# Kernel tuning notes

Hardware: AMD Instinct MI355X
Metric: run time of the kernel (lower is better)

Reference implementation:

```python
import jax, jax.numpy as jnp
import numpy as np

HID = 128


def setup_inputs() -> dict:
    key = jax.random.key(0)
    ks = jax.random.split(key, 7)
    B = 131072
    X = jax.random.normal(ks[0], (B, 4), dtype=jnp.float32)
    # Linear params stored as (in, out); scaled ~ 1/sqrt(fan_in) like torch default
    W1 = jax.random.normal(ks[1], (4, HID), dtype=jnp.float32) * 0.5
    b1 = jnp.zeros((HID,), jnp.float32)
    W2 = jax.random.normal(ks[2], (HID, HID), dtype=jnp.float32) * (1.0 / np.sqrt(HID))
    b2 = jnp.zeros((HID,), jnp.float32)
    W3 = jax.random.normal(ks[3], (HID, 1), dtype=jnp.float32) * (1.0 / np.sqrt(HID))
    b3 = jnp.zeros((1,), jnp.float32)
    return {"X": X, "W1": W1, "b1": b1, "W2": W2, "b2": b2, "W3": W3, "b3": b3}


def reference(X, W1, b1, W2, b2, W3, b3):
    def V_fn(feat):  # feat: [4] -> scalar potential
        h = jnp.tanh(feat @ W1 + b1)
        h = jnp.tanh(h @ W2 + b2)
        return (h @ W3 + b3)[0]

    def L_single(q, qd):  # q:[2], qd:[2] -> scalar Lagrangian
        t1, t2 = q[0], q[1]
        w1, w2 = qd[0], qd[1]
        T = w1 ** 2 + 0.5 * w2 ** 2 + w1 * w2 * jnp.cos(t1 - t2)
        feat = jnp.stack([jnp.sin(t1), jnp.cos(t1), jnp.sin(t2), jnp.cos(t2)])
        return T - V_fn(feat)

    q = X[:, :2]
    qd = X[:, 2:]
    dL_dq = jax.vmap(jax.grad(L_single, argnums=0))(q, qd)          # [B,2]
    # mass matrix M[i,j] = d^2 L / (d qd_i d qd_j)
    M = jax.vmap(jax.jacfwd(jax.grad(L_single, argnums=1), argnums=1))(q, qd)  # [B,2,2]
    # cross Hessian H[i,j] = d^2 L / (d qd_i d q_j); Coriolis C_i = H[i,:] @ qd
    H = jax.vmap(jax.jacfwd(jax.grad(L_single, argnums=1), argnums=0))(q, qd)  # [B,2,2]
    C = jnp.einsum('bij,bj->bi', H, qd)                              # [B,2]
    qdd = jnp.linalg.solve(M, (dL_dq - C)[..., None])[..., 0]        # [B,2]
    return jnp.concatenate([qd, qdd], axis=1)                        # [B,4]
```

## Files before the change

kernel.cpp:

```cpp
#include <hip/hip_runtime.h>
#include <math.h>

#define HID 128
#define SPB 64
#define TPB 512
#define GRIDB 512

typedef __bf16 bf16;
typedef bf16 bf16x8 __attribute__((ext_vector_type(8)));
typedef bf16 bf16x4 __attribute__((ext_vector_type(4)));
typedef float floatx4 __attribute__((ext_vector_type(4)));

__device__ __forceinline__ float fast_tanh(float x) {
    float e = __builtin_amdgcn_exp2f(x * 2.885390081777927f);
    return 1.0f - 2.0f * __builtin_amdgcn_rcpf(e + 1.0f);
}


__global__ __launch_bounds__(TPB, 4)
void lnn_kernel(const float* __restrict__ X,
                const float* __restrict__ W1,
                const float* __restrict__ b1,
                const float* __restrict__ b2,
                const float* __restrict__ W3,
                const float* __restrict__ W2,
                float* __restrict__ out,
                int B, int nchunk)
{
    __shared__ __align__(16) bf16 sW2A[16384];
    __shared__ __align__(16) bf16 sH1 [8192];
    __shared__ __align__(16) bf16 sG2 [8192];
    __shared__ __align__(16) float4 sW1c[HID];
    __shared__ float sB1[HID], sB2[HID], sW3[HID];
    __shared__ __align__(16) float sFeat[2][SPB][4];
    __shared__ float sQd[2][SPB][2];
    __shared__ __align__(16) float sDV[4][SPB][4];

    const int tid  = threadIdx.x;
    const int w    = tid >> 6;
    const int lane = tid & 63;
    const int lrow = lane & 15;
    const int lq   = lane >> 4;
    const int wlo  = w & 3;
    const int whi  = w >> 2;

    if (tid < HID) {
        sW1c[tid] = make_float4(W1[tid], W1[HID + tid], W1[2*HID + tid], W1[3*HID + tid]);
        sB1[tid]  = b1[tid];
    } else if (tid < 2 * HID) {
        sB2[tid - HID] = b2[tid - HID];
        sW3[tid - HID] = W3[tid - HID];
    }
    #pragma unroll
    for (int tt = 0; tt < 4; ++tt) {
        int e = tid + tt * TPB;
        int t = e >> 6, l = e & 63;
        int jt = t >> 2, kt = t & 3;
        int lr = l & 15, q = l >> 4;
        bf16x8 f;
        #pragma unroll
        for (int idx = 0; idx < 8; ++idx)
            f[idx] = (bf16)W2[(32*kt + 8*q + idx) * HID + 16*jt + lr];
        *reinterpret_cast<bf16x8*>(&sW2A[e * 8]) = f;
    }
    bf16x8 bW1 = {};
    if (lrow < 4) {
        const float4* wp = reinterpret_cast<const float4*>(&W1[lrow*HID + 32*wlo + 8*lq]);
        float4 a = wp[0], b = wp[1];
        bW1[0]=(bf16)a.x; bW1[1]=(bf16)a.y; bW1[2]=(bf16)a.z; bW1[3]=(bf16)a.w;
        bW1[4]=(bf16)b.x; bW1[5]=(bf16)b.y; bW1[6]=(bf16)b.z; bW1[7]=(bf16)b.w;
    }
    bf16x8 aW2[2][4];
    #pragma unroll
    for (int u = 0; u < 2; ++u) {
        const float* rbase = &W2[(16*(2*wlo + u) + lrow) * HID + 8*lq];
        #pragma unroll
        for (int jt2 = 0; jt2 < 4; ++jt2) {
            const float4* rp = reinterpret_cast<const float4*>(rbase + 32*jt2);
            float4 r0 = rp[0], r1 = rp[1];
            bf16x8 g;
            g[0]=(bf16)r0.x; g[1]=(bf16)r0.y; g[2]=(bf16)r0.z; g[3]=(bf16)r0.w;
            g[4]=(bf16)r1.x; g[5]=(bf16)r1.y; g[6]=(bf16)r1.z; g[7]=(bf16)r1.w;
            aW2[u][jt2] = g;
        }
    }
    if (tid >= TPB - SPB) {
        int s  = tid - (TPB - SPB);
        int g  = (int)blockIdx.x * SPB + s;
        int gc = g < B ? g : (B - 1);
        float4 x = reinterpret_cast<const float4*>(X)[gc];
        float s1, c1, s2, c2;
        __sincosf(x.x, &s1, &c1);
        __sincosf(x.y, &s2, &c2);
        sFeat[0][s][0]=s1; sFeat[0][s][1]=c1; sFeat[0][s][2]=s2; sFeat[0][s][3]=c2;
        sQd[0][s][0]=x.z;  sQd[0][s][1]=x.w;
    }
    __syncthreads();

    #pragma unroll 1
    for (int c = 0; c < nchunk; ++c) {
        const int par = c & 1;
        const int s0  = (c * GRIDB + (int)blockIdx.x) * SPB;

        {
            int s = 16 * wlo + lrow;
            float f0 = sFeat[par][s][0], f1 = sFeat[par][s][1];
            float f2 = sFeat[par][s][2], f3 = sFeat[par][s][3];
            #pragma unroll
            for (int h = 0; h < 2; ++h) {
                int kt = 2 * whi + h;
                int jb = 32 * kt + 8 * lq;
                float4 t0 = *reinterpret_cast<const float4*>(&sB1[jb]);
                float4 t1 = *reinterpret_cast<const float4*>(&sB1[jb + 4]);
                float bias[8] = {t0.x,t0.y,t0.z,t0.w,t1.x,t1.y,t1.z,t1.w};
                bf16x8 hf;
                #pragma unroll
                for (int idx = 0; idx < 8; ++idx) {
                    float4 wc = sW1c[jb + idx];
                    float z = bias[idx] + f0*wc.x + f1*wc.y + f2*wc.z + f3*wc.w;
                    hf[idx] = (bf16)fast_tanh(z);
                }
                *reinterpret_cast<bf16x8*>(&sH1[((wlo*4 + kt)*64 + lane)*8]) = hf;
            }
        }
        __syncthreads();

        floatx4 acc[2][2];
        #pragma unroll
        for (int t = 0; t < 2; ++t)
            #pragma unroll
            for (int s = 0; s < 2; ++s) acc[t][s] = floatx4{0.f,0.f,0.f,0.f};
        #pragma unroll
        for (int kt = 0; kt < 4; ++kt) {
            bf16x8 a0 = *reinterpret_cast<const bf16x8*>(&sW2A[(((2*wlo  )*4 + kt)*64 + lane)*8]);
            bf16x8 a1 = *reinterpret_cast<const bf16x8*>(&sW2A[(((2*wlo+1)*4 + kt)*64 + lane)*8]);
            bf16x8 b0 = *reinterpret_cast<const bf16x8*>(&sH1 [(((2*whi  )*4 + kt)*64 + lane)*8]);
            bf16x8 b1 = *reinterpret_cast<const bf16x8*>(&sH1 [(((2*whi+1)*4 + kt)*64 + lane)*8]);
            acc[0][0] = __builtin_amdgcn_mfma_f32_16x16x32_bf16(a0, b0, acc[0][0], 0,0,0);
            acc[0][1] = __builtin_amdgcn_mfma_f32_16x16x32_bf16(a0, b1, acc[0][1], 0,0,0);
            acc[1][0] = __builtin_amdgcn_mfma_f32_16x16x32_bf16(a1, b0, acc[1][0], 0,0,0);
            acc[1][1] = __builtin_amdgcn_mfma_f32_16x16x32_bf16(a1, b1, acc[1][1], 0,0,0);
        }

        #pragma unroll
        for (int t = 0; t < 2; ++t) {
            int jb = 16*(2*wlo + t) + 4*lq;
            float4 b2v = *reinterpret_cast<const float4*>(&sB2[jb]);
            float4 w3v = *reinterpret_cast<const float4*>(&sW3[jb]);
            float bbv[4] = {b2v.x, b2v.y, b2v.z, b2v.w};
            float w3a[4] = {w3v.x, w3v.y, w3v.z, w3v.w};
            int q2  = 2*t + (lq >> 1);
            int sub = 4 * (lq & 1);
            #pragma unroll
            for (int s = 0; s < 2; ++s) {
                int st = 2*whi + s;
                bf16x4 g;
                #pragma unroll
                for (int r = 0; r < 4; ++r) {
                    float h = fast_tanh(acc[t][s][r] + bbv[r]);
                    g[r] = (bf16)((1.0f - h*h) * w3a[r]);
                }
                *reinterpret_cast<bf16x4*>(&sG2[((st*4 + wlo)*64 + (q2*16 + lrow))*8 + sub]) = g;
            }
        }
        __syncthreads();

        #pragma unroll
        for (int t = 0; t < 2; ++t)
            #pragma unroll
            for (int s = 0; s < 2; ++s) acc[t][s] = floatx4{0.f,0.f,0.f,0.f};
        #pragma unroll
        for (int jt2 = 0; jt2 < 4; ++jt2) {
            bf16x8 g0 = *reinterpret_cast<const bf16x8*>(&sG2[(((2*whi  )*4 + jt2)*64 + lane)*8]);
            bf16x8 g1 = *reinterpret_cast<const bf16x8*>(&sG2[(((2*whi+1)*4 + jt2)*64 + lane)*8]);
            acc[0][0] = __builtin_amdgcn_mfma_f32_16x16x32_bf16(aW2[0][jt2], g0, acc[0][0], 0,0,0);
            acc[0][1] = __builtin_amdgcn_mfma_f32_16x16x32_bf16(aW2[0][jt2], g1, acc[0][1], 0,0,0);
            acc[1][0] = __builtin_amdgcn_mfma_f32_16x16x32_bf16(aW2[1][jt2], g0, acc[1][0], 0,0,0);
            acc[1][1] = __builtin_amdgcn_mfma_f32_16x16x32_bf16(aW2[1][jt2], g1, acc[1][1], 0,0,0);
        }

        #pragma unroll
        for (int u = 0; u < 2; ++u) {
            int q2  = 2*u + (lq >> 1);
            int sub = 4 * (lq & 1);
            #pragma unroll
            for (int s = 0; s < 2; ++s) {
                int st  = 2*whi + s;
                int off = ((st*4 + wlo)*64 + (q2*16 + lrow))*8 + sub;
                bf16x4 h4 = *reinterpret_cast<const bf16x4*>(&sH1[off]);
                bf16x4 g;
                #pragma unroll
                for (int r = 0; r < 4; ++r) {
                    float h1 = (float)h4[r];
                    g[r] = (bf16)((1.0f - h1*h1) * acc[u][s][r]);
                }
                *reinterpret_cast<bf16x4*>(&sH1[off]) = g;
            }
        }

        if (tid >= TPB - SPB && c + 1 < nchunk) {
            int s  = tid - (TPB - SPB);
            int g  = ((c + 1) * GRIDB + (int)blockIdx.x) * SPB + s;
            int gc = g < B ? g : (B - 1);
            float4 x = reinterpret_cast<const float4*>(X)[gc];
            float s1, c1, s2, c2;
            __sincosf(x.x, &s1, &c1);
            __sincosf(x.y, &s2, &c2);
            int np = par ^ 1;
            sFeat[np][s][0]=s1; sFeat[np][s][1]=c1; sFeat[np][s][2]=s2; sFeat[np][s][3]=c2;
            sQd[np][s][0]=x.z;  sQd[np][s][1]=x.w;
        }

        {
            bf16x8 g0 = *reinterpret_cast<const bf16x8*>(&sH1[(((2*whi  )*4 + wlo)*64 + lane)*8]);
            bf16x8 g1 = *reinterpret_cast<const bf16x8*>(&sH1[(((2*whi+1)*4 + wlo)*64 + lane)*8]);
            floatx4 d0 = __builtin_amdgcn_mfma_f32_16x16x32_bf16(bW1, g0, floatx4{0.f,0.f,0.f,0.f}, 0,0,0);
            floatx4 d1 = __builtin_amdgcn_mfma_f32_16x16x32_bf16(bW1, g1, floatx4{0.f,0.f,0.f,0.f}, 0,0,0);
            if (lane < 16) {
                *reinterpret_cast<float4*>(&sDV[wlo][16*(2*whi  ) + lane][0]) =
                    make_float4(d0[0], d0[1], d0[2], d0[3]);
                *reinterpret_cast<float4*>(&sDV[wlo][16*(2*whi+1) + lane][0]) =
                    make_float4(d1[0], d1[1], d1[2], d1[3]);
            }
        }
        __syncthreads();

        if (tid < SPB) {
            int g = s0 + tid;
            if (g < B) {
                float4 d0 = *reinterpret_cast<const float4*>(&sDV[0][tid][0]);
                float4 d1 = *reinterpret_cast<const float4*>(&sDV[1][tid][0]);
                float4 d2 = *reinterpret_cast<const float4*>(&sDV[2][tid][0]);
                float4 d3 = *reinterpret_cast<const float4*>(&sDV[3][tid][0]);
                float dV0 = d0.x + d1.x + d2.x + d3.x;
                float dV1 = d0.y + d1.y + d2.y + d3.y;
                float dV2 = d0.z + d1.z + d2.z + d3.z;
                float dV3 = d0.w + d1.w + d2.w + d3.w;
                float s1 = sFeat[par][tid][0], c1 = sFeat[par][tid][1];
                float s2 = sFeat[par][tid][2], c2 = sFeat[par][tid][3];
                float w1 = sQd[par][tid][0],  w2 = sQd[par][tid][1];
                float cosD = c1 * c2 + s1 * s2;
                float sinD = s1 * c2 - c1 * s2;
                float dVt1 = dV0 * c1 - dV1 * s1;
                float dVt2 = dV2 * c2 - dV3 * s2;
                float sT = w1 * w2 * sinD;
                float cw = sinD * (w2 - w1);
                float rhs1 = (-sT - dVt1) - w2 * cw;
                float rhs2 = ( sT - dVt2) - w1 * cw;
                float det = 2.0f - cosD * cosD;
                float inv = __builtin_amdgcn_rcpf(det);
                float qdd1 = (rhs1 - cosD * rhs2) * inv;
                float qdd2 = (2.0f * rhs2 - cosD * rhs1) * inv;
                *reinterpret_cast<float4*>(&out[4 * g]) = make_float4(w1, w2, qdd1, qdd2);
            }
        }
    }
}

extern "C" void kernel_launch(void* const* d_in, const int* in_sizes, int n_in,
                              void* d_out, int out_size, void* d_ws, size_t ws_size,
                              hipStream_t stream) {
    const float* X  = (const float*)d_in[0];
    const float* W1 = (const float*)d_in[1];
    const float* b1 = (const float*)d_in[2];
    const float* W2 = (const float*)d_in[3];
    const float* b2 = (const float*)d_in[4];
    const float* W3 = (const float*)d_in[5];
    float* out = (float*)d_out;
    int B = in_sizes[0] / 4;
    int nchunk = (B + GRIDB * SPB - 1) / (GRIDB * SPB);
    lnn_kernel<<<GRIDB, TPB, 0, stream>>>(X, W1, b1, b2, W3, W2, out, B, nchunk);
}
```

Baseline: 91.62 us.

## Hold W2 forward tiles in registers, alias LDS buffers, raise grid and occupancy

The transposed W2 A-fragments are loaded from LDS into registers once before the chunk loop, and the staging region is then reused for the H1 and G2 buffers, roughly halving shared-memory use. That makes room for a larger grid (768 blocks) and a launch_bounds minimum of 6 blocks per CU, which should improve latency hiding. W1 is stored row-major so the layer-1 and tanh work can be expressed as float4 vector operations. The risk is register pressure: 16 bf16x8 weight fragments held per thread under a tighter register cap could cause spills.

```diff
diff --git a/kernel.cpp b/kernel.cpp
--- a/kernel.cpp
+++ b/kernel.cpp
@@ -4,20 +4,25 @@
 #define HID 128
 #define SPB 64
 #define TPB 512
-#define GRIDB 512
+#define GRIDB 768
 
 typedef __bf16 bf16;
 typedef bf16 bf16x8 __attribute__((ext_vector_type(8)));
 typedef bf16 bf16x4 __attribute__((ext_vector_type(4)));
 typedef float floatx4 __attribute__((ext_vector_type(4)));
 
-__device__ __forceinline__ float fast_tanh(float x) {
-    float e = __builtin_amdgcn_exp2f(x * 2.885390081777927f);
-    return 1.0f - 2.0f * __builtin_amdgcn_rcpf(e + 1.0f);
+__device__ __forceinline__ floatx4 tanh4(floatx4 z) {
+    floatx4 t = z * 2.885390081777927f;
+    floatx4 e = { __builtin_amdgcn_exp2f(t[0]), __builtin_amdgcn_exp2f(t[1]),
+                  __builtin_amdgcn_exp2f(t[2]), __builtin_amdgcn_exp2f(t[3]) };
+    e = e + 1.0f;
+    floatx4 r = { __builtin_amdgcn_rcpf(e[0]), __builtin_amdgcn_rcpf(e[1]),
+                  __builtin_amdgcn_rcpf(e[2]), __builtin_amdgcn_rcpf(e[3]) };
+    return 1.0f - 2.0f * r;
 }
 
 
-__global__ __launch_bounds__(TPB, 4)
+__global__ __launch_bounds__(TPB, 6)
 void lnn_kernel(const float* __restrict__ X,
                 const float* __restrict__ W1,
                 const float* __restrict__ b1,
@@ -27,14 +32,15 @@
                 float* __restrict__ out,
                 int B, int nchunk)
 {
-    __shared__ __align__(16) bf16 sW2A[16384];
-    __shared__ __align__(16) bf16 sH1 [8192];
-    __shared__ __align__(16) bf16 sG2 [8192];
-    __shared__ __align__(16) float4 sW1c[HID];
-    __shared__ float sB1[HID], sB2[HID], sW3[HID];
+    __shared__ __align__(16) bf16 sBuf[16384];
+    __shared__ __align__(16) float sW1r[4][HID];
+    __shared__ __align__(16) float sB1[HID], sB2[HID], sW3[HID];
     __shared__ __align__(16) float sFeat[2][SPB][4];
     __shared__ float sQd[2][SPB][2];
     __shared__ __align__(16) float sDV[4][SPB][4];
+
+    bf16* const sH1 = sBuf;
+    bf16* const sG2 = sBuf + 8192;
 
     const int tid  = threadIdx.x;
     const int w    = tid >> 6;
@@ -44,13 +50,14 @@
     const int wlo  = w & 3;
     const int whi  = w >> 2;
 
-    if (tid < HID) {
-        sW1c[tid] = make_float4(W1[tid], W1[HID + tid], W1[2*HID + tid], W1[3*HID + tid]);
-        sB1[tid]  = b1[tid];
-    } else if (tid < 2 * HID) {
-        sB2[tid - HID] = b2[tid - HID];
-        sW3[tid - HID] = W3[tid - HID];
-    }
+    {
+        int r = tid >> 7, j = tid & (HID - 1);
+        sW1r[r][j] = W1[r * HID + j];
+    }
+    if (tid < HID) sB1[tid] = b1[tid];
+    else if (tid < 2 * HID) sB2[tid - HID] = b2[tid - HID];
+    else if (tid < 3 * HID) sW3[tid - 2 * HID] = W3[tid - 2 * HID];
+
     #pragma unroll
     for (int tt = 0; tt < 4; ++tt) {
         int e = tid + tt * TPB;
@@ -61,7 +68,7 @@
         #pragma unroll
         for (int idx = 0; idx < 8; ++idx)
             f[idx] = (bf16)W2[(32*kt + 8*q + idx) * HID + 16*jt + lr];
-        *reinterpret_cast<bf16x8*>(&sW2A[e * 8]) = f;
+        *reinterpret_cast<bf16x8*>(&sBuf[e * 8]) = f;
     }
     bf16x8 bW1 = {};
     if (lrow < 4) {
@@ -97,6 +104,14 @@
     }
     __syncthreads();
 
+    bf16x8 aW2T[2][4];
+    #pragma unroll
+    for (int u = 0; u < 2; ++u)
+        #pragma unroll
+        for (int kt = 0; kt < 4; ++kt)
+            aW2T[u][kt] = *reinterpret_cast<const bf16x8*>(&sBuf[(((2*wlo+u)*4 + kt)*64 + lane)*8]);
+    __syncthreads();
+
     #pragma unroll 1
     for (int c = 0; c < nchunk; ++c) {
         const int par = c & 1;
@@ -110,16 +125,23 @@
             for (int h = 0; h < 2; ++h) {
                 int kt = 2 * whi + h;
                 int jb = 32 * kt + 8 * lq;
-                float4 t0 = *reinterpret_cast<const float4*>(&sB1[jb]);
-                float4 t1 = *reinterpret_cast<const float4*>(&sB1[jb + 4]);
-                float bias[8] = {t0.x,t0.y,t0.z,t0.w,t1.x,t1.y,t1.z,t1.w};
+                floatx4 w0a = *reinterpret_cast<const floatx4*>(&sW1r[0][jb]);
+                floatx4 w0b = *reinterpret_cast<const floatx4*>(&sW1r[0][jb+4]);
+                floatx4 w1a = *reinterpret_cast<const floatx4*>(&sW1r[1][jb]);
+                floatx4 w1b = *reinterpret_cast<const floatx4*>(&sW1r[1][jb+4]);
+                floatx4 w2a = *reinterpret_cast<const floatx4*>(&sW1r[2][jb]);
+                floatx4 w2b = *reinterpret_cast<const floatx4*>(&sW1r[2][jb+4]);
+                floatx4 w3a = *reinterpret_cast<const floatx4*>(&sW1r[3][jb]);
+                floatx4 w3b = *reinterpret_cast<const floatx4*>(&sW1r[3][jb+4]);
+                floatx4 bba = *reinterpret_cast<const floatx4*>(&sB1[jb]);
+                floatx4 bbb = *reinterpret_cast<const floatx4*>(&sB1[jb+4]);
+                floatx4 za = bba + f0*w0a + f1*w1a + f2*w2a + f3*w3a;
+                floatx4 zb = bbb + f0*w0b + f1*w1b + f2*w2b + f3*w3b;
+                floatx4 ha = tanh4(za);
+                floatx4 hb = tanh4(zb);
                 bf16x8 hf;
-                #pragma unroll
-                for (int idx = 0; idx < 8; ++idx) {
-                    float4 wc = sW1c[jb + idx];
-                    float z = bias[idx] + f0*wc.x + f1*wc.y + f2*wc.z + f3*wc.w;
-                    hf[idx] = (bf16)fast_tanh(z);
-                }
+                hf[0]=(bf16)ha[0]; hf[1]=(bf16)ha[1]; hf[2]=(bf16)ha[2]; hf[3]=(bf16)ha[3];
+                hf[4]=(bf16)hb[0]; hf[5]=(bf16)hb[1]; hf[6]=(bf16)hb[2]; hf[7]=(bf16)hb[3];
                 *reinterpret_cast<bf16x8*>(&sH1[((wlo*4 + kt)*64 + lane)*8]) = hf;
             }
         }
@@ -132,34 +154,28 @@
             for (int s = 0; s < 2; ++s) acc[t][s] = floatx4{0.f,0.f,0.f,0.f};
         #pragma unroll
         for (int kt = 0; kt < 4; ++kt) {
-            bf16x8 a0 = *reinterpret_cast<const bf16x8*>(&sW2A[(((2*wlo  )*4 + kt)*64 + lane)*8]);
-            bf16x8 a1 = *reinterpret_cast<const bf16x8*>(&sW2A[(((2*wlo+1)*4 + kt)*64 + lane)*8]);
-            bf16x8 b0 = *reinterpret_cast<const bf16x8*>(&sH1 [(((2*whi  )*4 + kt)*64 + lane)*8]);
-            bf16x8 b1 = *reinterpret_cast<const bf16x8*>(&sH1 [(((2*whi+1)*4 + kt)*64 + lane)*8]);
-            acc[0][0] = __builtin_amdgcn_mfma_f32_16x16x32_bf16(a0, b0, acc[0][0], 0,0,0);
-            acc[0][1] = __builtin_amdgcn_mfma_f32_16x16x32_bf16(a0, b1, acc[0][1], 0,0,0);
-            acc[1][0] = __builtin_amdgcn_mfma_f32_16x16x32_bf16(a1, b0, acc[1][0], 0,0,0);
-            acc[1][1] = __builtin_amdgcn_mfma_f32_16x16x32_bf16(a1, b1, acc[1][1], 0,0,0);
+            bf16x8 b0 = *reinterpret_cast<const bf16x8*>(&sH1[(((2*whi  )*4 + kt)*64 + lane)*8]);
+            bf16x8 b1v = *reinterpret_cast<const bf16x8*>(&sH1[(((2*whi+1)*4 + kt)*64 + lane)*8]);
+            acc[0][0] = __builtin_amdgcn_mfma_f32_16x16x32_bf16(aW2T[0][kt], b0,  acc[0][0], 0,0,0);
+            acc[0][1] = __builtin_amdgcn_mfma_f32_16x16x32_bf16(aW2T[0][kt], b1v, acc[0][1], 0,0,0);
+            acc[1][0] = __builtin_amdgcn_mfma_f32_16x16x32_bf16(aW2T[1][kt], b0,  acc[1][0], 0,0,0);
+            acc[1][1] = __builtin_amdgcn_mfma_f32_16x16x32_bf16(aW2T[1][kt], b1v, acc[1][1], 0,0,0);
         }
 
         #pragma unroll
         for (int t = 0; t < 2; ++t) {
             int jb = 16*(2*wlo + t) + 4*lq;
-            float4 b2v = *reinterpret_cast<const float4*>(&sB2[jb]);
-            float4 w3v = *reinterpret_cast<const float4*>(&sW3[jb]);
-            float bbv[4] = {b2v.x, b2v.y, b2v.z, b2v.w};
-            float w3a[4] = {w3v.x, w3v.y, w3v.z, w3v.w};
+            floatx4 b2v = *reinterpret_cast<const floatx4*>(&sB2[jb]);
+            floatx4 w3v = *reinterpret_cast<const floatx4*>(&sW3[jb]);
             int q2  = 2*t + (lq >> 1);
             int sub = 4 * (lq & 1);
             #pragma unroll
             for (int s = 0; s < 2; ++s) {
                 int st = 2*whi + s;
+                floatx4 h = tanh4(acc[t][s] + b2v);
+                floatx4 gv = (1.0f - h*h) * w3v;
                 bf16x4 g;
-                #pragma unroll
-                for (int r = 0; r < 4; ++r) {
-                    float h = fast_tanh(acc[t][s][r] + bbv[r]);
-                    g[r] = (bf16)((1.0f - h*h) * w3a[r]);
-                }
+                g[0]=(bf16)gv[0]; g[1]=(bf16)gv[1]; g[2]=(bf16)gv[2]; g[3]=(bf16)gv[3];
                 *reinterpret_cast<bf16x4*>(&sG2[((st*4 + wlo)*64 + (q2*16 + lrow))*8 + sub]) = g;
             }
         }
@@ -188,12 +204,10 @@
                 int st  = 2*whi + s;
                 int off = ((st*4 + wlo)*64 + (q2*16 + lrow))*8 + sub;
                 bf16x4 h4 = *reinterpret_cast<const bf16x4*>(&sH1[off]);
+                floatx4 hf = { (float)h4[0], (float)h4[1], (float)h4[2], (float)h4[3] };
+                floatx4 gv = (1.0f - hf*hf) * acc[u][s];
                 bf16x4 g;
-                #pragma unroll
-                for (int r = 0; r < 4; ++r) {
-                    float h1 = (float)h4[r];
-                    g[r] = (bf16)((1.0f - h1*h1) * acc[u][s][r]);
-                }
+                g[0]=(bf16)gv[0]; g[1]=(bf16)gv[1]; g[2]=(bf16)gv[2]; g[3]=(bf16)gv[3];
                 *reinterpret_cast<bf16x4*>(&sH1[off]) = g;
             }
         }
@@ -228,21 +242,18 @@
         if (tid < SPB) {
             int g = s0 + tid;
             if (g < B) {
-                float4 d0 = *reinterpret_cast<const float4*>(&sDV[0][tid][0]);
-                float4 d1 = *reinterpret_cast<const float4*>(&sDV[1][tid][0]);
-                float4 d2 = *reinterpret_cast<const float4*>(&sDV[2][tid][0]);
-                float4 d3 = *reinterpret_cast<const float4*>(&sDV[3][tid][0]);
-                float dV0 = d0.x + d1.x + d2.x + d3.x;
-                float dV1 = d0.y + d1.y + d2.y + d3.y;
-                float dV2 = d0.z + d1.z + d2.z + d3.z;
-                float dV3 = d0.w + d1.w + d2.w + d3.w;
+                floatx4 d0 = *reinterpret_cast<const floatx4*>(&sDV[0][tid][0]);
+                floatx4 d1 = *reinterpret_cast<const floatx4*>(&sDV[1][tid][0]);
+                floatx4 d2 = *reinterpret_cast<const floatx4*>(&sDV[2][tid][0]);
+                floatx4 d3 = *reinterpret_cast<const floatx4*>(&sDV[3][tid][0]);
+                floatx4 dV = (d0 + d1) + (d2 + d3);
                 float s1 = sFeat[par][tid][0], c1 = sFeat[par][tid][1];
                 float s2 = sFeat[par][tid][2], c2 = sFeat[par][tid][3];
                 float w1 = sQd[par][tid][0],  w2 = sQd[par][tid][1];
                 float cosD = c1 * c2 + s1 * s2;
                 float sinD = s1 * c2 - c1 * s2;
-                float dVt1 = dV0 * c1 - dV1 * s1;
-                float dVt2 = dV2 * c2 - dV3 * s2;
+                float dVt1 = dV[0] * c1 - dV[1] * s1;
+                float dVt2 = dV[2] * c2 - dV[3] * s2;
                 float sT = w1 * w2 * sinD;
                 float cw = sinD * (w2 - w1);
                 float rhs1 = (-sT - dVt1) - w2 * cw;
```

Result: slower. 134.1 us (+46.4%).
